# Performance work log

Measured on AMD Instinct MI355X. Metric: run time of the kernel, lower is better.

Reference implementation:

```python
import jax, jax.numpy as jnp
import numpy as np

N = 1024      # number of residues/tokens
D = 768       # node feature dim (heads * d_head)
H = 12        # heads
DH = D // H   # d_head = 64
DP = 128      # pair feature dim
SCALE = 0.125 # 1/sqrt(d_head)
EPS = 1e-5

def _ln(x, w, b):
    m = jnp.mean(x, axis=-1, keepdims=True)
    v = jnp.var(x, axis=-1, keepdims=True)
    return (x - m) * jax.lax.rsqrt(v + EPS) * w + b

def setup_inputs() -> dict:
    key = jax.random.key(0)
    ks = jax.random.split(key, 8)
    s = 0.02
    return {
        "node_feats": jax.random.normal(ks[0], (N, D), dtype=jnp.float32),
        "pair_feats": jax.random.normal(ks[1], (N, N, DP), dtype=jnp.float32),
        "ln_node_w": jnp.ones((D,), jnp.float32), "ln_node_b": jnp.zeros((D,), jnp.float32),
        "pair_ln_w": jnp.ones((DP,), jnp.float32), "pair_ln_b": jnp.zeros((DP,), jnp.float32),
        "qkv_W": jax.random.normal(ks[2], (D, 3 * D), dtype=jnp.float32) * s,
        "qkv_b": jnp.zeros((3 * D,), jnp.float32),
        "q_ln_w": jnp.ones((D,), jnp.float32), "q_ln_b": jnp.zeros((D,), jnp.float32),
        "k_ln_w": jnp.ones((D,), jnp.float32), "k_ln_b": jnp.zeros((D,), jnp.float32),
        "g_W": jax.random.normal(ks[3], (D, D), dtype=jnp.float32) * s,
        "g_b": jnp.zeros((D,), jnp.float32),
        "bias_W": jax.random.normal(ks[4], (DP, H), dtype=jnp.float32) * s,
        "bias_b": jnp.zeros((H,), jnp.float32),
        "out_W": jax.random.normal(ks[5], (D, D), dtype=jnp.float32) * s,
        "out_b": jnp.zeros((D,), jnp.float32),
        "mask": jax.random.bernoulli(ks[6], 0.9, (N, N)),
    }

def reference(node_feats, pair_feats, ln_node_w, ln_node_b, pair_ln_w, pair_ln_b,
              qkv_W, qkv_b, q_ln_w, q_ln_b, k_ln_w, k_ln_b,
              g_W, g_b, bias_W, bias_b, out_W, out_b, mask):
    x = _ln(node_feats, ln_node_w, ln_node_b)                 # [N, D]
    p = _ln(pair_feats, pair_ln_w, pair_ln_b)                 # [N, N, DP]
    q, k, v = jnp.split(x @ qkv_W + qkv_b, 3, axis=-1)        # each [N, D]
    q = _ln(q, q_ln_w, q_ln_b)
    k = _ln(k, k_ln_w, k_ln_b)
    g = x @ g_W + g_b                                         # [N, D]
    bias = jnp.einsum('ijp,ph->hij', p, bias_W) + bias_b[:, None, None]  # [H, N, N]
    bias = bias + jnp.where(mask[None, :, :], 0.0, -10000.0)
    q = q.reshape(N, H, DH); k = k.reshape(N, H, DH); v = v.reshape(N, H, DH)
    logits = jnp.einsum('ihd,jhd->hij', q, k) * SCALE + bias  # [H, N, N]
    attn = jax.nn.softmax(logits, axis=-1)
    out = jnp.einsum('hij,jhd->ihd', attn, v).reshape(N, D)   # [N, D]
    out = jax.nn.sigmoid(g) * out
    return out @ out_W + out_b
```

## Files before the change

kernel.cpp:

```cpp
#include <hip/hip_runtime.h>
#include <math.h>

#define N_TOK 1024
#define D_DIM 768
#define H_N   12
#define DH    64
#define DP    128
#define SCALE 0.125f
#define EPS   1e-5f
#define NN    (N_TOK * N_TOK)

__global__ __launch_bounds__(128) void prep_kernel(
    const float* __restrict__ pair_ln_w, const float* __restrict__ pair_ln_b,
    const float* __restrict__ bias_W, const float* __restrict__ bias_b,
    float* __restrict__ W2, float* __restrict__ S2cb)
{
    __shared__ float Ws[DP * H_N];
    __shared__ float slw[DP], slb[DP];
    int t = threadIdx.x;
    slw[t] = pair_ln_w[t];
    slb[t] = pair_ln_b[t];
    for (int idx = t; idx < DP * H_N; idx += 128) Ws[idx] = bias_W[idx];
    __syncthreads();
    for (int idx = t; idx < DP * H_N; idx += 128) {
        int c = idx / H_N;
        W2[idx] = slw[c] * Ws[idx];
    }
    if (t < 24) {
        int h = t % H_N;
        bool isS = t < H_N;
        float s = 0.f;
        for (int c = 0; c < DP; ++c)
            s += (isS ? slw[c] : slb[c]) * Ws[c * H_N + h];
        S2cb[t] = isS ? s : (s + bias_b[h]);
    }
}

__global__ __launch_bounds__(256) void ln_kernel(
    const float* __restrict__ in, float* __restrict__ out,
    int istride, int ostride,
    const float* __restrict__ w, const float* __restrict__ b)
{
    int row = blockIdx.x;
    int tid = threadIdx.x;
    const float* ip = in + (size_t)row * istride;
    float v0 = ip[tid], v1 = ip[tid + 256], v2 = ip[tid + 512];
    float s = v0 + v1 + v2;
    float q = v0 * v0 + v1 * v1 + v2 * v2;
    __shared__ float red[8];
    #pragma unroll
    for (int o = 32; o > 0; o >>= 1) {
        s += __shfl_down(s, o);
        q += __shfl_down(q, o);
    }
    int lane = tid & 63, wv = tid >> 6;
    if (lane == 0) { red[wv] = s; red[4 + wv] = q; }
    __syncthreads();
    if (tid == 0) {
        float ss = red[0] + red[1] + red[2] + red[3];
        float qq = red[4] + red[5] + red[6] + red[7];
        float mean = ss * (1.f / 768.f);
        float var = qq * (1.f / 768.f) - mean * mean;
        red[0] = mean;
        red[1] = rsqrtf(var + EPS);
    }
    __syncthreads();
    float mean = red[0], rstd = red[1];
    float* op = out + (size_t)row * ostride;
    op[tid]       = (v0 - mean) * rstd * w[tid]       + b[tid];
    op[tid + 256] = (v1 - mean) * rstd * w[tid + 256] + b[tid + 256];
    op[tid + 512] = (v2 - mean) * rstd * w[tid + 512] + b[tid + 512];
}

__global__ __launch_bounds__(256) void sgemm(
    const float* __restrict__ A, int lda,
    const float* __restrict__ B0, int ldb0, const float* __restrict__ bias0,
    const float* __restrict__ B1, int ldb1, const float* __restrict__ bias1,
    int split, float* __restrict__ C, int ldc, int K)
{
    __shared__ __align__(16) float As[16 * 68];
    __shared__ __align__(16) float Bs[16 * 132];
    int tid = threadIdx.x;
    int tx = tid & 15, ty = tid >> 4;
    int m0 = blockIdx.y * 64, n0 = blockIdx.x * 128;
    const float* Bp; const float* bp; int ldb, bcol0;
    if (n0 < split) { Bp = B0; bp = bias0; ldb = ldb0; bcol0 = n0; }
    else            { Bp = B1; bp = bias1; ldb = ldb1; bcol0 = n0 - split; }

    float acc[4][8] = {};
    int ar = tid >> 2, ak = (tid & 3) * 4;
    int bk = tid >> 5, bc = (tid & 31) * 4;

    for (int kt = 0; kt < K; kt += 16) {
        float4 av  = *(const float4*)&A[(size_t)(m0 + ar) * lda + kt + ak];
        float4 b0v = *(const float4*)&Bp[(size_t)(kt + bk) * ldb + bcol0 + bc];
        float4 b1v = *(const float4*)&Bp[(size_t)(kt + bk + 8) * ldb + bcol0 + bc];
        As[(ak + 0) * 68 + ar] = av.x;
        As[(ak + 1) * 68 + ar] = av.y;
        As[(ak + 2) * 68 + ar] = av.z;
        As[(ak + 3) * 68 + ar] = av.w;
        *(float4*)&Bs[bk * 132 + bc] = b0v;
        *(float4*)&Bs[(bk + 8) * 132 + bc] = b1v;
        __syncthreads();
        #pragma unroll
        for (int kk = 0; kk < 16; ++kk) {
            float4 a  = *(const float4*)&As[kk * 68 + ty * 4];
            float4 b0 = *(const float4*)&Bs[kk * 132 + tx * 4];
            float4 b1 = *(const float4*)&Bs[kk * 132 + 64 + tx * 4];
            float av_[4] = { a.x, a.y, a.z, a.w };
            float bv_[8] = { b0.x, b0.y, b0.z, b0.w, b1.x, b1.y, b1.z, b1.w };
            #pragma unroll
            for (int u = 0; u < 4; ++u)
                #pragma unroll
                for (int i = 0; i < 8; ++i)
                    acc[u][i] += av_[u] * bv_[i];
        }
        __syncthreads();
    }
    float4 bb0 = *(const float4*)&bp[bcol0 + tx * 4];
    float4 bb1 = *(const float4*)&bp[bcol0 + 64 + tx * 4];
    #pragma unroll
    for (int u = 0; u < 4; ++u) {
        float* cp = &C[(size_t)(m0 + ty * 4 + u) * ldc + n0];
        float4 o0, o1;
        o0.x = acc[u][0] + bb0.x; o0.y = acc[u][1] + bb0.y;
        o0.z = acc[u][2] + bb0.z; o0.w = acc[u][3] + bb0.w;
        o1.x = acc[u][4] + bb1.x; o1.y = acc[u][5] + bb1.y;
        o1.z = acc[u][6] + bb1.z; o1.w = acc[u][7] + bb1.w;
        *(float4*)&cp[tx * 4]      = o0;
        *(float4*)&cp[64 + tx * 4] = o1;
    }
}

__global__ __launch_bounds__(256) void bias_kernel(
    const float* __restrict__ pair, const int* __restrict__ mask,
    const float* __restrict__ W2, const float* __restrict__ S2cb,
    float* __restrict__ biasbuf)
{
    __shared__ __align__(16) float4 Lp[64 * 32];
    __shared__ __align__(16) float sW2[DP * H_N];
    __shared__ float sS[H_N], sC[H_N];
    int tid = threadIdx.x;
    for (int t = tid; t < DP * H_N; t += 256) sW2[t] = W2[t];
    if (tid < H_N) { sS[tid] = S2cb[tid]; sC[tid] = S2cb[H_N + tid]; }

    int r = tid >> 2, qq = tid & 3;
    const float4* pair4 = (const float4*)pair;

    for (int c = 0; c < 4; ++c) {
        int gid0 = (blockIdx.x * 4 + c) * 64;
        __syncthreads();
        #pragma unroll
        for (int i = 0; i < 8; ++i) {
            int n = i * 256 + tid;
            int row = n >> 5, c4 = n & 31;
            Lp[row * 32 + ((c4 + 2 * row) & 31)] = pair4[(size_t)gid0 * 32 + n];
        }
        __syncthreads();

        float sum = 0.f, ssq = 0.f;
        float dot[H_N];
        #pragma unroll
        for (int h = 0; h < H_N; ++h) dot[h] = 0.f;

        #pragma unroll
        for (int i = 0; i < 8; ++i) {
            int c4 = qq + 4 * i;
            float4 v = Lp[r * 32 + ((c4 + 2 * r) & 31)];
            float e[4] = { v.x, v.y, v.z, v.w };
            #pragma unroll
            for (int k = 0; k < 4; ++k) {
                float x = e[k];
                sum += x; ssq += x * x;
                const float4* wp4 = (const float4*)&sW2[(c4 * 4 + k) * H_N];
                float4 w0 = wp4[0], w1 = wp4[1], w2 = wp4[2];
                dot[0] += x * w0.x; dot[1] += x * w0.y; dot[2]  += x * w0.z; dot[3]  += x * w0.w;
                dot[4] += x * w1.x; dot[5] += x * w1.y; dot[6]  += x * w1.z; dot[7]  += x * w1.w;
                dot[8] += x * w2.x; dot[9] += x * w2.y; dot[10] += x * w2.z; dot[11] += x * w2.w;
            }
        }
        #pragma unroll
        for (int o = 1; o < 4; o <<= 1) {
            sum += __shfl_xor(sum, o);
            ssq += __shfl_xor(ssq, o);
            #pragma unroll
            for (int h = 0; h < H_N; ++h) dot[h] += __shfl_xor(dot[h], o);
        }
        float mean = sum * (1.f / 128.f);
        float var  = ssq * (1.f / 128.f) - mean * mean;
        float rstd = rsqrtf(var + EPS);
        float mz = (mask[gid0 + r] != 0) ? 0.f : -10000.f;
        #pragma unroll
        for (int s = 0; s < 3; ++s) {
            int h = qq * 3 + s;
            biasbuf[(size_t)h * NN + gid0 + r] = (dot[h] - mean * sS[h]) * rstd + sC[h] + mz;
        }
    }
}

__global__ __launch_bounds__(256) void attn_kernel(
    const float* __restrict__ xw, const float* __restrict__ biasbuf,
    float* __restrict__ attn_out)
{
    const int h  = blockIdx.y;
    const int i0 = blockIdx.x * 16;
    const int tid = threadIdx.x;

    __shared__ __align__(16) float Qs[16 * 68];
    __shared__ __align__(16) float Ks[64 * 64];
    __shared__ __align__(16) float Vs[64 * 68];
    __shared__ float Ps[16 * 68];
    __shared__ float alrow[16], lfin[16];

    {
        int r = tid >> 4, c4 = tid & 15;
        float4 v = *(const float4*)(xw + (size_t)(i0 + r) * 3072 + h * 64 + c4 * 4);
        float* d = &Qs[r * 68 + c4 * 4];
        d[0] = v.x * SCALE; d[1] = v.y * SCALE; d[2] = v.z * SCALE; d[3] = v.w * SCALE;
    }

    const int tj = tid & 31, tq = tid >> 5;
    const float* q0p = &Qs[(2 * tq) * 68];
    const float* q1p = q0p + 68;
    const float* k0p = &Ks[(2 * tj) << 6];
    const float* k1p = k0p + 64;
    const int swz = tj & 7;
    const float* brow0 = biasbuf + (size_t)h * NN + (size_t)(i0 + 2 * tq) * N_TOK;
    const float* brow1 = brow0 + N_TOK;
    const int tx = tid & 15, ty = tid >> 4;

    float m0r = -1e30f, m1r = -1e30f, l0 = 0.f, l1 = 0.f;
    float a0 = 0.f, a1 = 0.f, a2 = 0.f, a3 = 0.f;

    for (int j0 = 0; j0 < N_TOK; j0 += 64) {
        #pragma unroll
        for (int q2 = 0; q2 < 4; ++q2) {
            int idx = q2 * 256 + tid;
            int rr = idx >> 4, c4 = idx & 15;
            const float* gp = xw + (size_t)(j0 + rr) * 3072 + 768 + h * 64 + c4 * 4;
            float4 kv = *(const float4*)gp;
            *(float4*)&Ks[(rr << 6) + ((c4 ^ ((rr >> 1) & 7)) << 2)] = kv;
            float4 vv = *(const float4*)(gp + 768);
            *(float4*)&Vs[rr * 68 + c4 * 4] = vv;
        }
        __syncthreads();

        float4 s00 = {0,0,0,0}, s01 = {0,0,0,0}, s10 = {0,0,0,0}, s11 = {0,0,0,0};
        #pragma unroll
        for (int d4 = 0; d4 < 16; ++d4) {
            float4 qa = *(const float4*)&q0p[d4 << 2];
            float4 qb = *(const float4*)&q1p[d4 << 2];
            int o = (d4 ^ swz) << 2;
            float4 ka = *(const float4*)&k0p[o];
            float4 kb = *(const float4*)&k1p[o];
            s00.x += qa.x * ka.x; s00.y += qa.y * ka.y; s00.z += qa.z * ka.z; s00.w += qa.w * ka.w;
            s01.x += qa.x * kb.x; s01.y += qa.y * kb.y; s01.z += qa.z * kb.z; s01.w += qa.w * kb.w;
            s10.x += qb.x * ka.x; s10.y += qb.y * ka.y; s10.z += qb.z * ka.z; s10.w += qb.w * ka.w;
            s11.x += qb.x * kb.x; s11.y += qb.y * kb.y; s11.z += qb.z * kb.z; s11.w += qb.w * kb.w;
        }
        float2 b0 = *(const float2*)&brow0[j0 + 2 * tj];
        float2 b1 = *(const float2*)&brow1[j0 + 2 * tj];
        float S00 = s00.x + s00.y + s00.z + s00.w + b0.x;
        float S01 = s01.x + s01.y + s01.z + s01.w + b0.y;
        float S10 = s10.x + s10.y + s10.z + s10.w + b1.x;
        float S11 = s11.x + s11.y + s11.z + s11.w + b1.y;

        float mt0 = fmaxf(S00, S01), mt1 = fmaxf(S10, S11);
        #pragma unroll
        for (int o = 1; o < 32; o <<= 1) {
            mt0 = fmaxf(mt0, __shfl_xor(mt0, o));
            mt1 = fmaxf(mt1, __shfl_xor(mt1, o));
        }
        float mn0 = fmaxf(m0r, mt0), mn1 = fmaxf(m1r, mt1);
        float al0 = __expf(m0r - mn0), al1 = __expf(m1r - mn1);
        float p00 = __expf(S00 - mn0), p01 = __expf(S01 - mn0);
        float p10 = __expf(S10 - mn1), p11 = __expf(S11 - mn1);
        float rs0 = p00 + p01, rs1 = p10 + p11;
        #pragma unroll
        for (int o = 1; o < 32; o <<= 1) {
            rs0 += __shfl_xor(rs0, o);
            rs1 += __shfl_xor(rs1, o);
        }
        l0 = l0 * al0 + rs0; l1 = l1 * al1 + rs1;
        m0r = mn0; m1r = mn1;
        *(float2*)&Ps[(2 * tq) * 68 + 2 * tj]     = make_float2(p00, p01);
        *(float2*)&Ps[(2 * tq + 1) * 68 + 2 * tj] = make_float2(p10, p11);
        if (tj == 0) { alrow[2 * tq] = al0; alrow[2 * tq + 1] = al1; }
        __syncthreads();

        float als = alrow[ty];
        a0 *= als; a1 *= als; a2 *= als; a3 *= als;
        const float* prow = &Ps[ty * 68];
        #pragma unroll
        for (int j = 0; j < 64; ++j) {
            float pv = prow[j];
            float4 vv = *(const float4*)&Vs[j * 68 + tx * 4];
            a0 += pv * vv.x; a1 += pv * vv.y; a2 += pv * vv.z; a3 += pv * vv.w;
        }
        __syncthreads();
    }

    if (tj == 0) { lfin[2 * tq] = l0; lfin[2 * tq + 1] = l1; }
    __syncthreads();

    float inv = 1.f / lfin[ty];
    int row = i0 + ty;
    float4 gv = *(const float4*)(xw + (size_t)row * 3072 + 2304 + h * 64 + tx * 4);
    float* op = attn_out + (size_t)row * 768 + h * 64 + tx * 4;
    op[0] = a0 * inv / (1.f + __expf(-gv.x));
    op[1] = a1 * inv / (1.f + __expf(-gv.y));
    op[2] = a2 * inv / (1.f + __expf(-gv.z));
    op[3] = a3 * inv / (1.f + __expf(-gv.w));
}

extern "C" void kernel_launch(void* const* d_in, const int* in_sizes, int n_in,
                              void* d_out, int out_size, void* d_ws, size_t ws_size,
                              hipStream_t stream)
{
    const float* node      = (const float*)d_in[0];
    const float* pair      = (const float*)d_in[1];
    const float* ln_node_w = (const float*)d_in[2];
    const float* ln_node_b = (const float*)d_in[3];
    const float* pair_ln_w = (const float*)d_in[4];
    const float* pair_ln_b = (const float*)d_in[5];
    const float* qkv_W     = (const float*)d_in[6];
    const float* qkv_b     = (const float*)d_in[7];
    const float* q_ln_w    = (const float*)d_in[8];
    const float* q_ln_b    = (const float*)d_in[9];
    const float* k_ln_w    = (const float*)d_in[10];
    const float* k_ln_b    = (const float*)d_in[11];
    const float* g_W       = (const float*)d_in[12];
    const float* g_b       = (const float*)d_in[13];
    const float* bias_W    = (const float*)d_in[14];
    const float* bias_b    = (const float*)d_in[15];
    const float* out_W     = (const float*)d_in[16];
    const float* out_b     = (const float*)d_in[17];
    const int*   mask      = (const int*)d_in[18];
    float* out = (float*)d_out;

    float* ws      = (float*)d_ws;
    float* x       = ws;
    float* xw      = x + 786432;
    float* W2      = xw + 3145728;
    float* S2cb    = W2 + 1536;
    float* biasbuf = S2cb + 32;
    float* attn_o  = biasbuf + 12582912;

    prep_kernel<<<1, 128, 0, stream>>>(pair_ln_w, pair_ln_b, bias_W, bias_b, W2, S2cb);
    ln_kernel<<<1024, 256, 0, stream>>>(node, x, 768, 768, ln_node_w, ln_node_b);
    sgemm<<<dim3(24, 16), 256, 0, stream>>>(x, 768,
                                            qkv_W, 2304, qkv_b,
                                            g_W, 768, g_b,
                                            2304, xw, 3072, 768);
    ln_kernel<<<1024, 256, 0, stream>>>(xw, xw, 3072, 3072, q_ln_w, q_ln_b);
    ln_kernel<<<1024, 256, 0, stream>>>(xw + 768, xw + 768, 3072, 3072, k_ln_w, k_ln_b);
    bias_kernel<<<4096, 256, 0, stream>>>(pair, mask, W2, S2cb, biasbuf);
    attn_kernel<<<dim3(64, 12), 256, 0, stream>>>(xw, biasbuf, attn_o);
    sgemm<<<dim3(6, 16), 256, 0, stream>>>(attn_o, 768,
                                           out_W, 768, out_b,
                                           out_W, 768, out_b,
                                           1 << 30, out, 768, 768);
}
```

Measured before the change: 1.033 ms.

## Merge QKV GEMM with pair-bias kernel, prefetch tiles, fuse Q/K LN, retile out GEMM

Folds the QKV/gate GEMM and the pair-bias kernel into one launch that branches on block index, so the small GEMM's 384 blocks run alongside the bandwidth-heavy pair-bias blocks. Register prefetching of the next tile is added to the GEMM, the bias kernel and the attention K/V loads, so global loads overlap compute. The two Q/K layernorm launches become one kernel, and the output GEMM moves to 64x64 tiles to launch more blocks. In exchange there is higher register pressure and a larger shared-memory footprint in the merged kernel, which may reduce occupancy.

```diff
diff --git a/kernel.cpp b/kernel.cpp
--- a/kernel.cpp
+++ b/kernel.cpp
@@ -72,128 +72,187 @@
     op[tid + 512] = (v2 - mean) * rstd * w[tid + 512] + b[tid + 512];
 }
 
-__global__ __launch_bounds__(256) void sgemm(
-    const float* __restrict__ A, int lda,
-    const float* __restrict__ B0, int ldb0, const float* __restrict__ bias0,
-    const float* __restrict__ B1, int ldb1, const float* __restrict__ bias1,
-    int split, float* __restrict__ C, int ldc, int K)
-{
-    __shared__ __align__(16) float As[16 * 68];
-    __shared__ __align__(16) float Bs[16 * 132];
+__global__ __launch_bounds__(256) void qkln_kernel(
+    float* __restrict__ xw,
+    const float* __restrict__ qw, const float* __restrict__ qb,
+    const float* __restrict__ kw, const float* __restrict__ kb)
+{
+    int row = blockIdx.x >> 1, sel = blockIdx.x & 1;
     int tid = threadIdx.x;
-    int tx = tid & 15, ty = tid >> 4;
-    int m0 = blockIdx.y * 64, n0 = blockIdx.x * 128;
-    const float* Bp; const float* bp; int ldb, bcol0;
-    if (n0 < split) { Bp = B0; bp = bias0; ldb = ldb0; bcol0 = n0; }
-    else            { Bp = B1; bp = bias1; ldb = ldb1; bcol0 = n0 - split; }
-
-    float acc[4][8] = {};
-    int ar = tid >> 2, ak = (tid & 3) * 4;
-    int bk = tid >> 5, bc = (tid & 31) * 4;
-
-    for (int kt = 0; kt < K; kt += 16) {
-        float4 av  = *(const float4*)&A[(size_t)(m0 + ar) * lda + kt + ak];
-        float4 b0v = *(const float4*)&Bp[(size_t)(kt + bk) * ldb + bcol0 + bc];
-        float4 b1v = *(const float4*)&Bp[(size_t)(kt + bk + 8) * ldb + bcol0 + bc];
-        As[(ak + 0) * 68 + ar] = av.x;
-        As[(ak + 1) * 68 + ar] = av.y;
-        As[(ak + 2) * 68 + ar] = av.z;
-        As[(ak + 3) * 68 + ar] = av.w;
-        *(float4*)&Bs[bk * 132 + bc] = b0v;
-        *(float4*)&Bs[(bk + 8) * 132 + bc] = b1v;
-        __syncthreads();
-        #pragma unroll
-        for (int kk = 0; kk < 16; ++kk) {
-            float4 a  = *(const float4*)&As[kk * 68 + ty * 4];
-            float4 b0 = *(const float4*)&Bs[kk * 132 + tx * 4];
-            float4 b1 = *(const float4*)&Bs[kk * 132 + 64 + tx * 4];
-            float av_[4] = { a.x, a.y, a.z, a.w };
-            float bv_[8] = { b0.x, b0.y, b0.z, b0.w, b1.x, b1.y, b1.z, b1.w };
-            #pragma unroll
-            for (int u = 0; u < 4; ++u)
-                #pragma unroll
-                for (int i = 0; i < 8; ++i)
-                    acc[u][i] += av_[u] * bv_[i];
-        }
-        __syncthreads();
-    }
-    float4 bb0 = *(const float4*)&bp[bcol0 + tx * 4];
-    float4 bb1 = *(const float4*)&bp[bcol0 + 64 + tx * 4];
+    float* p = xw + (size_t)row * 3072 + sel * 768;
+    const float* w = sel ? kw : qw;
+    const float* b = sel ? kb : qb;
+    float v0 = p[tid], v1 = p[tid + 256], v2 = p[tid + 512];
+    float s = v0 + v1 + v2;
+    float q = v0 * v0 + v1 * v1 + v2 * v2;
+    __shared__ float red[8];
     #pragma unroll
-    for (int u = 0; u < 4; ++u) {
-        float* cp = &C[(size_t)(m0 + ty * 4 + u) * ldc + n0];
-        float4 o0, o1;
-        o0.x = acc[u][0] + bb0.x; o0.y = acc[u][1] + bb0.y;
-        o0.z = acc[u][2] + bb0.z; o0.w = acc[u][3] + bb0.w;
-        o1.x = acc[u][4] + bb1.x; o1.y = acc[u][5] + bb1.y;
-        o1.z = acc[u][6] + bb1.z; o1.w = acc[u][7] + bb1.w;
-        *(float4*)&cp[tx * 4]      = o0;
-        *(float4*)&cp[64 + tx * 4] = o1;
-    }
-}
-
-__global__ __launch_bounds__(256) void bias_kernel(
+    for (int o = 32; o > 0; o >>= 1) {
+        s += __shfl_down(s, o);
+        q += __shfl_down(q, o);
+    }
+    int lane = tid & 63, wv = tid >> 6;
+    if (lane == 0) { red[wv] = s; red[4 + wv] = q; }
+    __syncthreads();
+    if (tid == 0) {
+        float ss = red[0] + red[1] + red[2] + red[3];
+        float qq = red[4] + red[5] + red[6] + red[7];
+        float mean = ss * (1.f / 768.f);
+        float var = qq * (1.f / 768.f) - mean * mean;
+        red[0] = mean;
+        red[1] = rsqrtf(var + EPS);
+    }
+    __syncthreads();
+    float mean = red[0], rstd = red[1];
+    p[tid]       = (v0 - mean) * rstd * w[tid]       + b[tid];
+    p[tid + 256] = (v1 - mean) * rstd * w[tid + 256] + b[tid + 256];
+    p[tid + 512] = (v2 - mean) * rstd * w[tid + 512] + b[tid + 512];
+}
+
+__global__ __launch_bounds__(256) void mega_kernel(
+    const float* __restrict__ x,
+    const float* __restrict__ qkv_W, const float* __restrict__ qkv_b,
+    const float* __restrict__ g_W, const float* __restrict__ g_b,
+    float* __restrict__ xw,
     const float* __restrict__ pair, const int* __restrict__ mask,
     const float* __restrict__ W2, const float* __restrict__ S2cb,
     float* __restrict__ biasbuf)
 {
-    __shared__ __align__(16) float4 Lp[64 * 32];
-    __shared__ __align__(16) float sW2[DP * H_N];
-    __shared__ float sS[H_N], sC[H_N];
+    __shared__ __align__(16) char smem[39040];
     int tid = threadIdx.x;
-    for (int t = tid; t < DP * H_N; t += 256) sW2[t] = W2[t];
-    if (tid < H_N) { sS[tid] = S2cb[tid]; sC[tid] = S2cb[H_N + tid]; }
-
-    int r = tid >> 2, qq = tid & 3;
-    const float4* pair4 = (const float4*)pair;
-
-    for (int c = 0; c < 4; ++c) {
-        int gid0 = (blockIdx.x * 4 + c) * 64;
-        __syncthreads();
-        #pragma unroll
-        for (int i = 0; i < 8; ++i) {
-            int n = i * 256 + tid;
-            int row = n >> 5, c4 = n & 31;
-            Lp[row * 32 + ((c4 + 2 * row) & 31)] = pair4[(size_t)gid0 * 32 + n];
-        }
-        __syncthreads();
-
-        float sum = 0.f, ssq = 0.f;
-        float dot[H_N];
-        #pragma unroll
-        for (int h = 0; h < H_N; ++h) dot[h] = 0.f;
-
-        #pragma unroll
-        for (int i = 0; i < 8; ++i) {
-            int c4 = qq + 4 * i;
-            float4 v = Lp[r * 32 + ((c4 + 2 * r) & 31)];
-            float e[4] = { v.x, v.y, v.z, v.w };
-            #pragma unroll
-            for (int k = 0; k < 4; ++k) {
-                float x = e[k];
-                sum += x; ssq += x * x;
-                const float4* wp4 = (const float4*)&sW2[(c4 * 4 + k) * H_N];
-                float4 w0 = wp4[0], w1 = wp4[1], w2 = wp4[2];
-                dot[0] += x * w0.x; dot[1] += x * w0.y; dot[2]  += x * w0.z; dot[3]  += x * w0.w;
-                dot[4] += x * w1.x; dot[5] += x * w1.y; dot[6]  += x * w1.z; dot[7]  += x * w1.w;
-                dot[8] += x * w2.x; dot[9] += x * w2.y; dot[10] += x * w2.z; dot[11] += x * w2.w;
-            }
-        }
-        #pragma unroll
-        for (int o = 1; o < 4; o <<= 1) {
-            sum += __shfl_xor(sum, o);
-            ssq += __shfl_xor(ssq, o);
-            #pragma unroll
-            for (int h = 0; h < H_N; ++h) dot[h] += __shfl_xor(dot[h], o);
-        }
-        float mean = sum * (1.f / 128.f);
-        float var  = ssq * (1.f / 128.f) - mean * mean;
-        float rstd = rsqrtf(var + EPS);
-        float mz = (mask[gid0 + r] != 0) ? 0.f : -10000.f;
-        #pragma unroll
-        for (int s = 0; s < 3; ++s) {
-            int h = qq * 3 + s;
-            biasbuf[(size_t)h * NN + gid0 + r] = (dot[h] - mean * sS[h]) * rstd + sC[h] + mz;
+
+    if (blockIdx.x < 384) {
+        float* As = (float*)smem;
+        float* Bs = (float*)(smem + 4352);
+        int bid = blockIdx.x;
+        int tx = tid & 15, ty = tid >> 4;
+        int m0 = (bid / 24) * 64, n0 = (bid % 24) * 128;
+        const float* Bp; const float* bp; int ldb, bcol0;
+        if (n0 < 2304) { Bp = qkv_W; bp = qkv_b; ldb = 2304; bcol0 = n0; }
+        else           { Bp = g_W;   bp = g_b;   ldb = 768;  bcol0 = n0 - 2304; }
+
+        float acc[4][8] = {};
+        int ar = tid >> 2, ak = (tid & 3) * 4;
+        int bk = tid >> 5, bc = (tid & 31) * 4;
+
+        float4 av  = *(const float4*)&x[(size_t)(m0 + ar) * 768 + ak];
+        float4 b0v = *(const float4*)&Bp[(size_t)bk * ldb + bcol0 + bc];
+        float4 b1v = *(const float4*)&Bp[(size_t)(bk + 8) * ldb + bcol0 + bc];
+
+        for (int kt = 0; kt < 768; kt += 16) {
+            As[(ak + 0) * 68 + ar] = av.x;
+            As[(ak + 1) * 68 + ar] = av.y;
+            As[(ak + 2) * 68 + ar] = av.z;
+            As[(ak + 3) * 68 + ar] = av.w;
+            *(float4*)&Bs[bk * 132 + bc] = b0v;
+            *(float4*)&Bs[(bk + 8) * 132 + bc] = b1v;
+            __syncthreads();
+            if (kt + 16 < 768) {
+                av  = *(const float4*)&x[(size_t)(m0 + ar) * 768 + kt + 16 + ak];
+                b0v = *(const float4*)&Bp[(size_t)(kt + 16 + bk) * ldb + bcol0 + bc];
+                b1v = *(const float4*)&Bp[(size_t)(kt + 24 + bk) * ldb + bcol0 + bc];
+            }
+            #pragma unroll
+            for (int kk = 0; kk < 16; ++kk) {
+                float4 a  = *(const float4*)&As[kk * 68 + ty * 4];
+                float4 b0 = *(const float4*)&Bs[kk * 132 + tx * 4];
+                float4 b1 = *(const float4*)&Bs[kk * 132 + 64 + tx * 4];
+                float av_[4] = { a.x, a.y, a.z, a.w };
+                float bv_[8] = { b0.x, b0.y, b0.z, b0.w, b1.x, b1.y, b1.z, b1.w };
+                #pragma unroll
+                for (int u = 0; u < 4; ++u)
+                    #pragma unroll
+                    for (int i = 0; i < 8; ++i)
+                        acc[u][i] += av_[u] * bv_[i];
+            }
+            __syncthreads();
+        }
+        float4 bb0 = *(const float4*)&bp[bcol0 + tx * 4];
+        float4 bb1 = *(const float4*)&bp[bcol0 + 64 + tx * 4];
+        #pragma unroll
+        for (int u = 0; u < 4; ++u) {
+            float* cp = &xw[(size_t)(m0 + ty * 4 + u) * 3072 + n0];
+            float4 o0, o1;
+            o0.x = acc[u][0] + bb0.x; o0.y = acc[u][1] + bb0.y;
+            o0.z = acc[u][2] + bb0.z; o0.w = acc[u][3] + bb0.w;
+            o1.x = acc[u][4] + bb1.x; o1.y = acc[u][5] + bb1.y;
+            o1.z = acc[u][6] + bb1.z; o1.w = acc[u][7] + bb1.w;
+            *(float4*)&cp[tx * 4]      = o0;
+            *(float4*)&cp[64 + tx * 4] = o1;
+        }
+    } else {
+        float4* Lp  = (float4*)smem;
+        float*  sW2 = (float*)(smem + 32768);
+        float*  sS  = (float*)(smem + 38912);
+        float*  sC  = (float*)(smem + 38960);
+        int bb = blockIdx.x - 384;
+
+        for (int t = tid; t < DP * H_N; t += 256) sW2[t] = W2[t];
+        if (tid < H_N) { sS[tid] = S2cb[tid]; sC[tid] = S2cb[H_N + tid]; }
+
+        int r = tid >> 2, qq = tid & 3;
+        const float4* pair4 = (const float4*)pair;
+
+        float4 pv[8];
+        {
+            size_t base = (size_t)(bb * 4) * 64 * 32;
+            #pragma unroll
+            for (int i = 0; i < 8; ++i) pv[i] = pair4[base + i * 256 + tid];
+        }
+
+        for (int c = 0; c < 4; ++c) {
+            int gid0 = (bb * 4 + c) * 64;
+            __syncthreads();
+            #pragma unroll
+            for (int i = 0; i < 8; ++i) {
+                int n = i * 256 + tid;
+                int row = n >> 5, c4 = n & 31;
+                Lp[row * 32 + ((c4 + 2 * row) & 31)] = pv[i];
+            }
+            __syncthreads();
+            if (c < 3) {
+                size_t base = (size_t)(gid0 + 64) * 32;
+                #pragma unroll
+                for (int i = 0; i < 8; ++i) pv[i] = pair4[base + i * 256 + tid];
+            }
+
+            float sum = 0.f, ssq = 0.f;
+            float dot[H_N];
+            #pragma unroll
+            for (int h = 0; h < H_N; ++h) dot[h] = 0.f;
+
+            #pragma unroll
+            for (int i = 0; i < 8; ++i) {
+                int c4 = qq + 4 * i;
+                float4 v = Lp[r * 32 + ((c4 + 2 * r) & 31)];
+                float e[4] = { v.x, v.y, v.z, v.w };
+                #pragma unroll
+                for (int k = 0; k < 4; ++k) {
+                    float xx = e[k];
+                    sum += xx; ssq += xx * xx;
+                    const float4* wp4 = (const float4*)&sW2[(c4 * 4 + k) * H_N];
+                    float4 w0 = wp4[0], w1 = wp4[1], w2 = wp4[2];
+                    dot[0] += xx * w0.x; dot[1] += xx * w0.y; dot[2]  += xx * w0.z; dot[3]  += xx * w0.w;
+                    dot[4] += xx * w1.x; dot[5] += xx * w1.y; dot[6]  += xx * w1.z; dot[7]  += xx * w1.w;
+                    dot[8] += xx * w2.x; dot[9] += xx * w2.y; dot[10] += xx * w2.z; dot[11] += xx * w2.w;
+                }
+            }
+            #pragma unroll
+            for (int o = 1; o < 4; o <<= 1) {
+                sum += __shfl_xor(sum, o);
+                ssq += __shfl_xor(ssq, o);
+                #pragma unroll
+                for (int h = 0; h < H_N; ++h) dot[h] += __shfl_xor(dot[h], o);
+            }
+            float mean = sum * (1.f / 128.f);
+            float var  = ssq * (1.f / 128.f) - mean * mean;
+            float rstd = rsqrtf(var + EPS);
+            float mz = (mask[gid0 + r] != 0) ? 0.f : -10000.f;
+            #pragma unroll
+            for (int s = 0; s < 3; ++s) {
+                int h = qq * 3 + s;
+                biasbuf[(size_t)h * NN + gid0 + r] = (dot[h] - mean * sS[h]) * rstd + sC[h] + mz;
+            }
         }
     }
 }
@@ -229,21 +288,38 @@
     const float* brow1 = brow0 + N_TOK;
     const int tx = tid & 15, ty = tid >> 4;
 
+    const int srr = tid >> 4;
+    const int sc4 = tid & 15;
+
     float m0r = -1e30f, m1r = -1e30f, l0 = 0.f, l1 = 0.f;
     float a0 = 0.f, a1 = 0.f, a2 = 0.f, a3 = 0.f;
 
+    float4 kreg[4], vreg[4];
+    #pragma unroll
+    for (int q2 = 0; q2 < 4; ++q2) {
+        int rr = srr + q2 * 16;
+        const float* gp = xw + (size_t)rr * 3072 + 768 + h * 64 + sc4 * 4;
+        kreg[q2] = *(const float4*)gp;
+        vreg[q2] = *(const float4*)(gp + 768);
+    }
+
     for (int j0 = 0; j0 < N_TOK; j0 += 64) {
         #pragma unroll
         for (int q2 = 0; q2 < 4; ++q2) {
-            int idx = q2 * 256 + tid;
-            int rr = idx >> 4, c4 = idx & 15;
-            const float* gp = xw + (size_t)(j0 + rr) * 3072 + 768 + h * 64 + c4 * 4;
-            float4 kv = *(const float4*)gp;
-            *(float4*)&Ks[(rr << 6) + ((c4 ^ ((rr >> 1) & 7)) << 2)] = kv;
-            float4 vv = *(const float4*)(gp + 768);
-            *(float4*)&Vs[rr * 68 + c4 * 4] = vv;
+            int rr = srr + q2 * 16;
+            *(float4*)&Ks[(rr << 6) + ((sc4 ^ ((rr >> 1) & 7)) << 2)] = kreg[q2];
+            *(float4*)&Vs[rr * 68 + sc4 * 4] = vreg[q2];
         }
         __syncthreads();
+        if (j0 + 64 < N_TOK) {
+            #pragma unroll
+            for (int q2 = 0; q2 < 4; ++q2) {
+                int rr = srr + q2 * 16;
+                const float* gp = xw + (size_t)(j0 + 64 + rr) * 3072 + 768 + h * 64 + sc4 * 4;
+                kreg[q2] = *(const float4*)gp;
+                vreg[q2] = *(const float4*)(gp + 768);
+            }
+        }
 
         float4 s00 = {0,0,0,0}, s01 = {0,0,0,0}, s10 = {0,0,0,0}, s11 = {0,0,0,0};
         #pragma unroll
@@ -311,6 +387,55 @@
     op[1] = a1 * inv / (1.f + __expf(-gv.y));
     op[2] = a2 * inv / (1.f + __expf(-gv.z));
     op[3] = a3 * inv / (1.f + __expf(-gv.w));
+}
+
+__global__ __launch_bounds__(256) void sgemm64(
+    const float* __restrict__ A, const float* __restrict__ B,
+    const float* __restrict__ bias, float* __restrict__ C)
+{
+    __shared__ __align__(16) float As[16 * 68];
+    __shared__ __align__(16) float Bs[16 * 68];
+    int tid = threadIdx.x;
+    int tx = tid & 15, ty = tid >> 4;
+    int m0 = blockIdx.y * 64, n0 = blockIdx.x * 64;
+
+    float acc[4][4] = {};
+    int ar = tid >> 2, ak = (tid & 3) * 4;
+    int bk = tid >> 4, bc = (tid & 15) * 4;
+
+    float4 av = *(const float4*)&A[(size_t)(m0 + ar) * 768 + ak];
+    float4 bv = *(const float4*)&B[(size_t)bk * 768 + n0 + bc];
+
+    for (int kt = 0; kt < 768; kt += 16) {
+        As[(ak + 0) * 68 + ar] = av.x;
+        As[(ak + 1) * 68 + ar] = av.y;
+        As[(ak + 2) * 68 + ar] = av.z;
+        As[(ak + 3) * 68 + ar] = av.w;
+        *(float4*)&Bs[bk * 68 + bc] = bv;
+        __syncthreads();
+        if (kt + 16 < 768) {
+            av = *(const float4*)&A[(size_t)(m0 + ar) * 768 + kt + 16 + ak];
+            bv = *(const float4*)&B[(size_t)(kt + 16 + bk) * 768 + n0 + bc];
+        }
+        #pragma unroll
+        for (int kk = 0; kk < 16; ++kk) {
+            float4 a = *(const float4*)&As[kk * 68 + ty * 4];
+            float4 b = *(const float4*)&Bs[kk * 68 + tx * 4];
+            acc[0][0] += a.x * b.x; acc[0][1] += a.x * b.y; acc[0][2] += a.x * b.z; acc[0][3] += a.x * b.w;
+            acc[1][0] += a.y * b.x; acc[1][1] += a.y * b.y; acc[1][2] += a.y * b.z; acc[1][3] += a.y * b.w;
+            acc[2][0] += a.z * b.x; acc[2][1] += a.z * b.y; acc[2][2] += a.z * b.z; acc[2][3] += a.z * b.w;
+            acc[3][0] += a.w * b.x; acc[3][1] += a.w * b.y; acc[3][2] += a.w * b.z; acc[3][3] += a.w * b.w;
+        }
+        __syncthreads();
+    }
+    float4 bb = *(const float4*)&bias[n0 + tx * 4];
+    #pragma unroll
+    for (int u = 0; u < 4; ++u) {
+        float4 o;
+        o.x = acc[u][0] + bb.x; o.y = acc[u][1] + bb.y;
+        o.z = acc[u][2] + bb.z; o.w = acc[u][3] + bb.w;
+        *(float4*)&C[(size_t)(m0 + ty * 4 + u) * 768 + n0 + tx * 4] = o;
+    }
 }
 
 extern "C" void kernel_launch(void* const* d_in, const int* in_sizes, int n_in,
@@ -348,16 +473,9 @@
 
     prep_kernel<<<1, 128, 0, stream>>>(pair_ln_w, pair_ln_b, bias_W, bias_b, W2, S2cb);
     ln_kernel<<<1024, 256, 0, stream>>>(node, x, 768, 768, ln_node_w, ln_node_b);
-    sgemm<<<dim3(24, 16), 256, 0, stream>>>(x, 768,
-                                            qkv_W, 2304, qkv_b,
-                                            g_W, 768, g_b,
-                                            2304, xw, 3072, 768);
-    ln_kernel<<<1024, 256, 0, stream>>>(xw, xw, 3072, 3072, q_ln_w, q_ln_b);
-    ln_kernel<<<1024, 256, 0, stream>>>(xw + 768, xw + 768, 3072, 3072, k_ln_w, k_ln_b);
-    bias_kernel<<<4096, 256, 0, stream>>>(pair, mask, W2, S2cb, biasbuf);
+    mega_kernel<<<4480, 256, 0, stream>>>(x, qkv_W, qkv_b, g_W, g_b, xw,
+                                          pair, mask, W2, S2cb, biasbuf);
+    qkln_kernel<<<2048, 256, 0, stream>>>(xw, q_ln_w, q_ln_b, k_ln_w, k_ln_b);
     attn_kernel<<<dim3(64, 12), 256, 0, stream>>>(xw, biasbuf, attn_o);
-    sgemm<<<dim3(6, 16), 256, 0, stream>>>(attn_o, 768,
-                                           out_W, 768, out_b,
-                                           out_W, 768, out_b,
-                                           1 << 30, out, 768, 768);
-}
+    sgemm64<<<dim3(12, 16), 256, 0, stream>>>(attn_o, out_W, out_b, out);
+}
```

Measured after the change: 1.083 ms. 1.05x slower.
